# Kernel tuning notes

Hardware: AMD Instinct MI355X
Metric: run time of the kernel (lower is better)

The kernel has to match this reference:

```python
import jax, jax.numpy as jnp
import numpy as np

N = 100000
E = 1600000
IN_C = 128
OUT_C = 32
HEADS = 4
NEG_SLOPE = 0.2


def setup_inputs() -> dict:
    key = jax.random.key(0)
    k1, k2, k3, k4, k5 = jax.random.split(key, 5)
    x = jax.random.normal(k1, (N, IN_C), dtype=jnp.float32)
    edge_index = jax.random.randint(k2, (2, E), 0, N, dtype=jnp.int64)
    # Xavier-ish scaled params
    W = jax.random.normal(k3, (OUT_C * HEADS, IN_C), dtype=jnp.float32) * (1.414 * np.sqrt(2.0 / (IN_C + OUT_C * HEADS)))
    att_l = jax.random.normal(k4, (1, HEADS, OUT_C), dtype=jnp.float32) * 0.1
    att_r = jax.random.normal(k5, (1, HEADS, OUT_C), dtype=jnp.float32) * 0.1
    bias = jnp.zeros((OUT_C * HEADS,), dtype=jnp.float32)
    return {"x": x, "edge_index": edge_index, "W": W, "att_l": att_l, "att_r": att_r, "bias": bias}


def reference(x, edge_index, W, att_l, att_r, bias):
    row, col = edge_index[0], edge_index[1]
    # per-node projection: [N, H, C]
    x_proj = (x @ W.T).reshape(N, HEADS, OUT_C)
    x_i = x_proj[row]          # [E, H, C] gather by source
    x_j = x_proj[col]          # [E, H, C] gather by target
    alpha = (x_i * att_l).sum(-1) + (x_j * att_r).sum(-1)   # [E, H]
    alpha = jnp.where(alpha >= 0, alpha, NEG_SLOPE * alpha)  # leaky_relu
    # edge softmax grouped by row (faithful: plain exp, eps=1e-16)
    alpha_exp = jnp.exp(alpha)
    denom = jax.ops.segment_sum(alpha_exp, row, num_segments=N)  # [N, H]
    alpha = alpha_exp / (denom[row] + 1e-16)
    # weighted scatter-add over all heads at once: [N, H, C]
    out = jax.ops.segment_sum(x_j * alpha[:, :, None], row, num_segments=N)
    out = out.reshape(N, HEADS * OUT_C) + bias
    return out
```

## Files before the change

kernel.cpp:

```cpp
#include <hip/hip_runtime.h>
#include <hip/hip_fp16.h>


constexpr float NEG_SLOPE = 0.2f;
constexpr int TILE_ROWS = 64;
constexpr int SLAB = 2048;
constexpr int EPB = 8192;
constexpr int NB_PAD = 2048;
constexpr int FBMAX = 256;

typedef __attribute__((ext_vector_type(8))) short short8;
typedef __attribute__((ext_vector_type(4))) float f32x4;

__device__ inline short f2bf(float f) {
    unsigned u = __float_as_uint(f);
    return (short)((u + 0x7fffu + ((u >> 16) & 1u)) >> 16);
}

__global__ __launch_bounds__(256) void k_prep(const float* __restrict__ W,
                                              const float* __restrict__ attl,
                                              const float* __restrict__ attr,
                                              short* __restrict__ Wa) {
    int blk = blockIdx.x;
    int t = threadIdx.x;
    if (blk < 64) {
        int i = blk * 256 + t;
        Wa[i] = f2bf(W[i]);
    } else if (blk == 64) {
        for (int s = t; s < 1024; s += 256) {
            int which = s >> 9;
            int h = (s >> 7) & 3;
            int k = s & 127;
            const float* att = which ? attr : attl;
            float acc = 0.f;
#pragma unroll 8
            for (int c = 0; c < 32; ++c)
                acc += att[h * 32 + c] * W[(h * 32 + c) * 128 + k];
            Wa[(128 + which * 4 + h) * 128 + k] = f2bf(acc);
        }
    } else {
        int i = (blk - 65) * 256 + t;
        if (i < 1024) Wa[136 * 128 + i] = 0;
    }
}

__global__ __launch_bounds__(512) void k_fg(const float* __restrict__ x,
                                            const short* __restrict__ Wa,
                                            const int* __restrict__ ei,
                                            __half* __restrict__ xph,
                                            float* __restrict__ l,
                                            float* __restrict__ r,
                                            unsigned int* __restrict__ slab,
                                            int* __restrict__ starts,
                                            int N, int E, int NB, int FB) {
    __shared__ __align__(16) char smem[49152];
    __shared__ int s_wsum[8];
    int t = threadIdx.x;
    int lane = t & 63, wv = t >> 6;

    if ((int)blockIdx.x < FB) {
        int* s_hist = (int*)smem;
        int* s_cur  = (int*)(smem + 8192);
        unsigned int* s_stage = (unsigned int*)(smem + 16384);

        int fb = blockIdx.x;
        int e0 = fb * EPB;
        int ecnt = min(EPB, E - e0);
        bool full = (ecnt == EPB) && ((E & 3) == 0);

        for (int i = t; i < NB_PAD; i += 512) s_hist[i] = 0;
        __syncthreads();

        const int* rows = ei;
        const int* cols = ei + E;

        if (full) {
            const int4* r4 = (const int4*)rows + (e0 >> 2);
#pragma unroll
            for (int k = 0; k < 4; ++k) {
                int4 ra = r4[k * 512 + t];
                atomicAdd(&s_hist[ra.x >> 6], 1);
                atomicAdd(&s_hist[ra.y >> 6], 1);
                atomicAdd(&s_hist[ra.z >> 6], 1);
                atomicAdd(&s_hist[ra.w >> 6], 1);
            }
        } else {
            for (int j = t; j < ecnt; j += 512)
                atomicAdd(&s_hist[rows[e0 + j] >> 6], 1);
        }
        __syncthreads();

        int b0 = t * 4;
        int c0 = s_hist[b0], c1 = s_hist[b0 + 1], c2 = s_hist[b0 + 2], c3 = s_hist[b0 + 3];
        int p = c0 + c1 + c2 + c3;
        int v = p;
#pragma unroll
        for (int off = 1; off < 64; off <<= 1) {
            int u = __shfl_up(v, off);
            if (lane >= off) v += u;
        }
        if (lane == 63) s_wsum[wv] = v;
        __syncthreads();
        if (t == 0) {
            int run = 0;
#pragma unroll
            for (int w = 0; w < 8; ++w) { int tmp = s_wsum[w]; s_wsum[w] = run; run += tmp; }
        }
        __syncthreads();
        int base = s_wsum[wv] + (v - p);
        int e1 = base + c0, e2 = e1 + c1, e3 = e2 + c2;
        s_hist[b0] = base; s_hist[b0 + 1] = e1; s_hist[b0 + 2] = e2; s_hist[b0 + 3] = e3;
        s_cur[b0] = base;  s_cur[b0 + 1] = e1;  s_cur[b0 + 2] = e2;  s_cur[b0 + 3] = e3;
        size_t sb = (size_t)fb * (NB + 1);
        if (b0 + 0 <= NB) starts[sb + b0 + 0] = base;
        if (b0 + 1 <= NB) starts[sb + b0 + 1] = e1;
        if (b0 + 2 <= NB) starts[sb + b0 + 2] = e2;
        if (b0 + 3 <= NB) starts[sb + b0 + 3] = e3;
        __syncthreads();

        if (full) {
            const int4* r4 = (const int4*)rows + (e0 >> 2);
            const int4* c4 = (const int4*)cols + (e0 >> 2);
#pragma unroll
            for (int k = 0; k < 4; ++k) {
                int4 ra = r4[k * 512 + t];
                int4 ca = c4[k * 512 + t];
                int pos;
                pos = atomicAdd(&s_cur[ra.x >> 6], 1);
                s_stage[pos] = ((unsigned int)ca.x << 6) | (unsigned int)(ra.x & 63);
                pos = atomicAdd(&s_cur[ra.y >> 6], 1);
                s_stage[pos] = ((unsigned int)ca.y << 6) | (unsigned int)(ra.y & 63);
                pos = atomicAdd(&s_cur[ra.z >> 6], 1);
                s_stage[pos] = ((unsigned int)ca.z << 6) | (unsigned int)(ra.z & 63);
                pos = atomicAdd(&s_cur[ra.w >> 6], 1);
                s_stage[pos] = ((unsigned int)ca.w << 6) | (unsigned int)(ra.w & 63);
            }
        } else {
            for (int j = t; j < ecnt; j += 512) {
                int rr = rows[e0 + j], cc = cols[e0 + j];
                int pos = atomicAdd(&s_cur[rr >> 6], 1);
                s_stage[pos] = ((unsigned int)cc << 6) | (unsigned int)(rr & 63);
            }
        }
        __syncthreads();

        uint4* dst = (uint4*)(slab + (size_t)fb * EPB);
        const uint4* src = (const uint4*)s_stage;
        int n4 = (ecnt + 3) >> 2;
        for (int i = t; i < n4; i += 512) dst[i] = src[i];
        return;
    }

    short* s_wa = (short*)smem;
    {
        const short8* g = (const short8*)Wa;
        short8* s = (short8*)s_wa;
        for (int i = t; i < 144 * 16; i += 512) {
            int row = i >> 4, k8 = i & 15;
            s[row * 17 + k8] = g[i];
        }
    }
    __syncthreads();

    int li = lane & 15, quad = lane >> 4;
    int gb = blockIdx.x - FB;
    int base = gb * 128 + wv * 16;

    f32x4 acc[9];
#pragma unroll
    for (int nt = 0; nt < 9; ++nt) acc[nt] = (f32x4){0.f, 0.f, 0.f, 0.f};

    int anode = base + li;
    bool avalid = anode < N;
    const float4* x4 = (const float4*)x;
    const short8* wb8 = (const short8*)s_wa;

#pragma unroll
    for (int kc = 0; kc < 4; ++kc) {
        float4 p0 = make_float4(0.f, 0.f, 0.f, 0.f), p1 = p0;
        if (avalid) {
            p0 = x4[(size_t)anode * 32 + kc * 8 + quad * 2];
            p1 = x4[(size_t)anode * 32 + kc * 8 + quad * 2 + 1];
        }
        short8 a;
        a[0] = f2bf(p0.x); a[1] = f2bf(p0.y); a[2] = f2bf(p0.z); a[3] = f2bf(p0.w);
        a[4] = f2bf(p1.x); a[5] = f2bf(p1.y); a[6] = f2bf(p1.z); a[7] = f2bf(p1.w);
#pragma unroll
        for (int nt = 0; nt < 9; ++nt) {
            short8 b = wb8[(nt * 16 + li) * 17 + kc * 4 + quad];
            acc[nt] = __builtin_amdgcn_mfma_f32_16x16x32_bf16(a, b, acc[nt], 0, 0, 0);
        }
    }

#pragma unroll
    for (int j = 0; j < 4; ++j) {
        int node = base + quad * 4 + j;
        if (node >= N) continue;
        if (li < 4)      l[node * 4 + li] = acc[8][j];
        else if (li < 8) r[node * 4 + li - 4] = acc[8][j];
    }

    __syncthreads();
    __half* s_out = (__half*)s_wa;
#pragma unroll
    for (int j = 0; j < 4; ++j) {
        int nl = wv * 16 + quad * 4 + j;
#pragma unroll
        for (int nt = 0; nt < 8; ++nt)
            s_out[nl * 136 + nt * 16 + li] = __float2half(acc[nt][j]);
    }
    __syncthreads();
    {
        int nl = t >> 2, seg = t & 3;
        int node = gb * 128 + nl;
        if (node < N) {
            const short8* sr = (const short8*)s_wa;
            short8* xp8 = (short8*)xph;
#pragma unroll
            for (int q = 0; q < 4; ++q)
                xp8[(size_t)node * 16 + seg * 4 + q] = sr[nl * 17 + seg * 4 + q];
        }
    }
}

__global__ __launch_bounds__(512) void k_tile(const int* __restrict__ starts,
                                              const unsigned int* __restrict__ slab,
                                              const float* __restrict__ l,
                                              const float* __restrict__ r,
                                              const __half* __restrict__ xph,
                                              const float* __restrict__ bias,
                                              float* __restrict__ out,
                                              int N, int NB, int FB) {
    __shared__ unsigned int s_packed[SLAB];
    __shared__ int s_col[SLAB];
    __shared__ __half s_w[SLAB * 4];
    __shared__ float s_dsum[TILE_ROWS * 4];
    __shared__ float s_l[TILE_ROWS * 4];
    __shared__ int s_start[TILE_ROWS + 1];
    __shared__ int s_cursor[TILE_ROWS];
    __shared__ int s_cnt[TILE_ROWS];
    __shared__ int s_fbase[FBMAX];
    __shared__ int s_foff[FBMAX + 1];
    __shared__ int s_w4[4];

    int b = blockIdx.x;
    int base = b * TILE_ROWS;
    int t = threadIdx.x;
    int lane = t & 63, wv = t >> 6;
    int rows = min(TILE_ROWS, N - base);

    if (t < TILE_ROWS) s_cnt[t] = 0;
    if (t < rows * 4) s_l[t] = l[base * 4 + t];

    int myc = 0;
    if (t < FB) {
        const int* sp = starts + (size_t)t * (NB + 1) + b;
        int a0 = sp[0], a1 = sp[1];
        s_fbase[t] = a0;
        myc = a1 - a0;
    }
    int v = 0;
    if (t < 256) {
        v = myc;
#pragma unroll
        for (int off = 1; off < 64; off <<= 1) {
            int u = __shfl_up(v, off);
            if (lane >= off) v += u;
        }
        if (lane == 63) s_w4[wv] = v;
    }
    __syncthreads();
    if (t == 0) {
        int run = 0;
#pragma unroll
        for (int w = 0; w < 4; ++w) { int tmp = s_w4[w]; s_w4[w] = run; run += tmp; }
        s_foff[0] = 0;
    }
    __syncthreads();
    if (t < 256) s_foff[t + 1] = v + s_w4[wv];
    __syncthreads();
    int tot = s_foff[FB];
    if (tot > SLAB) tot = SLAB;

    for (int i = t; i < tot; i += 512) {
        int lo = 0, hi = FB;
        while (hi - lo > 1) {
            int mid = (lo + hi) >> 1;
            if (s_foff[mid] <= i) lo = mid; else hi = mid;
        }
        unsigned int p = slab[(size_t)lo * EPB + s_fbase[lo] + (i - s_foff[lo])];
        s_packed[i] = p;
        atomicAdd(&s_cnt[p & 63], 1);
    }
    __syncthreads();

    if (t < 64) {
        int c = s_cnt[t];
        int vv = c;
#pragma unroll
        for (int off = 1; off < 64; off <<= 1) {
            int u = __shfl_up(vv, off);
            if (t >= off) vv += u;
        }
        s_start[t + 1] = vv;
        if (t == 0) s_start[0] = 0;
        s_cursor[t] = vv - c;
    }
    __syncthreads();

    {
        int row_[4], col_[4];
        bool val_[4];
#pragma unroll
        for (int s = 0; s < 4; ++s) {
            int i = t + s * 512;
            bool valid = i < tot;
            unsigned int p = valid ? s_packed[i] : 0u;
            row_[s] = (int)(p & 63);
            col_[s] = valid ? (int)(p >> 6) : 0;
            val_[s] = valid;
        }
        float4 rv0 = ((const float4*)r)[col_[0]];
        float4 rv1 = ((const float4*)r)[col_[1]];
        float4 rv2 = ((const float4*)r)[col_[2]];
        float4 rv3 = ((const float4*)r)[col_[3]];
#pragma unroll
        for (int s = 0; s < 4; ++s) {
            if (!val_[s]) continue;
            float4 rv = s == 0 ? rv0 : s == 1 ? rv1 : s == 2 ? rv2 : rv3;
            int row = row_[s];
            int pos = atomicAdd(&s_cursor[row], 1);
            s_col[pos] = col_[s];
            float4 lv = ((const float4*)s_l)[row];
            float w0 = lv.x + rv.x, w1 = lv.y + rv.y;
            float w2 = lv.z + rv.z, w3 = lv.w + rv.w;
            w0 = w0 >= 0.f ? w0 : NEG_SLOPE * w0;
            w1 = w1 >= 0.f ? w1 : NEG_SLOPE * w1;
            w2 = w2 >= 0.f ? w2 : NEG_SLOPE * w2;
            w3 = w3 >= 0.f ? w3 : NEG_SLOPE * w3;
            w0 = __expf(w0); w1 = __expf(w1); w2 = __expf(w2); w3 = __expf(w3);
            ((__half2*)s_w)[pos * 2]     = __floats2half2_rn(w0, w1);
            ((__half2*)s_w)[pos * 2 + 1] = __floats2half2_rn(w2, w3);
        }
    }
    __syncthreads();

    if (t < 256) {
        int row = t >> 2, h = t & 3;
        if (row < rows) {
            int s0 = s_start[row], s1 = s_start[row + 1];
            float d = 0.f;
            for (int i = s0; i < s1; ++i)
                d += __half2float(s_w[i * 4 + h]);
            s_dsum[t] = d;
        }
    }
    __syncthreads();

    int quarter = lane >> 4;
    int li = lane & 15;
    int h = li >> 2;
    const float4* xp4g = (const float4*)xph;

    float4 b0 = ((const float4*)bias)[2 * li];
    float4 b1 = ((const float4*)bias)[2 * li + 1];

    for (int rl = wv; rl < rows; rl += 8) {
        int s0 = s_start[rl], s1 = s_start[rl + 1];
        float a0 = 0.f, a1 = 0.f, a2 = 0.f, a3 = 0.f;
        float a4 = 0.f, a5 = 0.f, a6 = 0.f, a7 = 0.f;
        for (int i = s0 + quarter; i < s1; i += 8) {
            int iB = i + 4;
            bool hB = iB < s1;
            int colA = s_col[i];
            float wA = __half2float(s_w[i * 4 + h]);
            int colB = hB ? s_col[iB] : colA;
            float wB = hB ? __half2float(s_w[iB * 4 + h]) : 0.f;
            float4 rawA = xp4g[(size_t)colA * 16 + li];
            float4 rawB = xp4g[(size_t)colB * 16 + li];
            {
                __half2* hp = (__half2*)&rawA;
                float2 f0 = __half22float2(hp[0]);
                float2 f1 = __half22float2(hp[1]);
                float2 f2 = __half22float2(hp[2]);
                float2 f3 = __half22float2(hp[3]);
                a0 += wA * f0.x; a1 += wA * f0.y;
                a2 += wA * f1.x; a3 += wA * f1.y;
                a4 += wA * f2.x; a5 += wA * f2.y;
                a6 += wA * f3.x; a7 += wA * f3.y;
            }
            {
                __half2* hp = (__half2*)&rawB;
                float2 f0 = __half22float2(hp[0]);
                float2 f1 = __half22float2(hp[1]);
                float2 f2 = __half22float2(hp[2]);
                float2 f3 = __half22float2(hp[3]);
                a0 += wB * f0.x; a1 += wB * f0.y;
                a2 += wB * f1.x; a3 += wB * f1.y;
                a4 += wB * f2.x; a5 += wB * f2.y;
                a6 += wB * f3.x; a7 += wB * f3.y;
            }
        }
        a0 += __shfl_xor(a0, 16); a0 += __shfl_xor(a0, 32);
        a1 += __shfl_xor(a1, 16); a1 += __shfl_xor(a1, 32);
        a2 += __shfl_xor(a2, 16); a2 += __shfl_xor(a2, 32);
        a3 += __shfl_xor(a3, 16); a3 += __shfl_xor(a3, 32);
        a4 += __shfl_xor(a4, 16); a4 += __shfl_xor(a4, 32);
        a5 += __shfl_xor(a5, 16); a5 += __shfl_xor(a5, 32);
        a6 += __shfl_xor(a6, 16); a6 += __shfl_xor(a6, 32);
        a7 += __shfl_xor(a7, 16); a7 += __shfl_xor(a7, 32);
        if (quarter == 0) {
            float inv = 1.f / (s_dsum[rl * 4 + h] + 1e-16f);
            float4 o0, o1;
            o0.x = a0 * inv + b0.x; o0.y = a1 * inv + b0.y;
            o0.z = a2 * inv + b0.z; o0.w = a3 * inv + b0.w;
            o1.x = a4 * inv + b1.x; o1.y = a5 * inv + b1.y;
            o1.z = a6 * inv + b1.z; o1.w = a7 * inv + b1.w;
            ((float4*)out)[(size_t)(base + rl) * 32 + 2 * li] = o0;
            ((float4*)out)[(size_t)(base + rl) * 32 + 2 * li + 1] = o1;
        }
    }
}

extern "C" void kernel_launch(void* const* d_in, const int* in_sizes, int n_in,
                              void* d_out, int out_size, void* d_ws, size_t ws_size,
                              hipStream_t stream) {
    const float* x    = (const float*)d_in[0];
    const int*   ei   = (const int*)d_in[1];
    const float* W    = (const float*)d_in[2];
    const float* attl = (const float*)d_in[3];
    const float* attr = (const float*)d_in[4];
    const float* bias = (const float*)d_in[5];
    int N = in_sizes[0] / 128;
    int E = in_sizes[1] / 2;
    int NB = (N + TILE_ROWS - 1) / TILE_ROWS;
    int FB = (E + EPB - 1) / EPB;

    char* ws = (char*)d_ws;
    __half* xph = (__half*)ws;   ws += (size_t)N * 128 * 2;
    float* l    = (float*)ws;    ws += (size_t)N * 4 * 4;
    float* r    = (float*)ws;    ws += (size_t)N * 4 * 4;
    short* Wa   = (short*)ws;    ws += 144 * 128 * 2;
    int* starts = (int*)ws;      ws += (size_t)FB * (NB + 1) * 4;
    unsigned int* slab = (unsigned int*)ws; ws += (size_t)FB * EPB * 4;

    float* out = (float*)d_out;
    int GB = (N + 127) / 128;

    k_prep<<<69, 256, 0, stream>>>(W, attl, attr, Wa);
    k_fg<<<FB + GB, 512, 0, stream>>>(x, Wa, ei, xph, l, r, slab, starts, N, E, NB, FB);
    k_tile<<<NB, 512, 0, stream>>>(starts, slab, l, r, xph, bias, out, N, NB, FB);
}
```

Measured before the change: 204.5 us.

## Fuse weight prep into fill/GEMM kernel, interleave fill blocks, unroll gather by four

Removes the separate k_prep launch. Every GEMM block now converts W to bf16 in shared memory and computes the attention-projected rows itself. Fill (bucketing) blocks are spread evenly among the GEMM blocks through a stride S instead of all being placed first, so the two kinds of work mix across CUs. The k_tile gather loop now issues four neighbour row loads per iteration instead of two, to raise memory-level parallelism. In exchange, every GEMM block redundantly reads all of W from global memory and computes the projected rows, which adds global traffic and ALU work per block.

```diff
diff --git a/kernel.cpp b/kernel.cpp
--- a/kernel.cpp
+++ b/kernel.cpp
@@ -17,53 +17,31 @@
     return (short)((u + 0x7fffu + ((u >> 16) & 1u)) >> 16);
 }
 
-__global__ __launch_bounds__(256) void k_prep(const float* __restrict__ W,
-                                              const float* __restrict__ attl,
-                                              const float* __restrict__ attr,
-                                              short* __restrict__ Wa) {
-    int blk = blockIdx.x;
-    int t = threadIdx.x;
-    if (blk < 64) {
-        int i = blk * 256 + t;
-        Wa[i] = f2bf(W[i]);
-    } else if (blk == 64) {
-        for (int s = t; s < 1024; s += 256) {
-            int which = s >> 9;
-            int h = (s >> 7) & 3;
-            int k = s & 127;
-            const float* att = which ? attr : attl;
-            float acc = 0.f;
-#pragma unroll 8
-            for (int c = 0; c < 32; ++c)
-                acc += att[h * 32 + c] * W[(h * 32 + c) * 128 + k];
-            Wa[(128 + which * 4 + h) * 128 + k] = f2bf(acc);
-        }
-    } else {
-        int i = (blk - 65) * 256 + t;
-        if (i < 1024) Wa[136 * 128 + i] = 0;
-    }
-}
-
 __global__ __launch_bounds__(512) void k_fg(const float* __restrict__ x,
-                                            const short* __restrict__ Wa,
+                                            const float* __restrict__ W,
+                                            const float* __restrict__ attl,
+                                            const float* __restrict__ attr,
                                             const int* __restrict__ ei,
                                             __half* __restrict__ xph,
                                             float* __restrict__ l,
                                             float* __restrict__ r,
                                             unsigned int* __restrict__ slab,
                                             int* __restrict__ starts,
-                                            int N, int E, int NB, int FB) {
+                                            int N, int E, int NB, int FB, int S) {
     __shared__ __align__(16) char smem[49152];
+    __shared__ float s_att[256];
     __shared__ int s_wsum[8];
     int t = threadIdx.x;
     int lane = t & 63, wv = t >> 6;
-
-    if ((int)blockIdx.x < FB) {
+    int b = blockIdx.x;
+    bool isfill = (b % S == 0) && (b / S < FB);
+
+    if (isfill) {
         int* s_hist = (int*)smem;
         int* s_cur  = (int*)(smem + 8192);
         unsigned int* s_stage = (unsigned int*)(smem + 16384);
 
-        int fb = blockIdx.x;
+        int fb = b / S;
         int e0 = fb * EPB;
         int ecnt = min(EPB, E - e0);
         bool full = (ecnt == EPB) && ((E & 3) == 0);
@@ -152,18 +130,33 @@
     }
 
     short* s_wa = (short*)smem;
-    {
-        const short8* g = (const short8*)Wa;
-        short8* s = (short8*)s_wa;
-        for (int i = t; i < 144 * 16; i += 512) {
-            int row = i >> 4, k8 = i & 15;
-            s[row * 17 + k8] = g[i];
-        }
+    if (t < 128)       s_att[t] = attl[t];
+    else if (t < 256)  s_att[t] = attr[t - 128];
+    for (int i = t; i < 128 * 128; i += 512) {
+        int row = i >> 7, col = i & 127;
+        s_wa[row * 136 + col] = f2bf(W[i]);
+    }
+    for (int i = t; i < 1024; i += 512) {
+        int row = 136 + (i >> 7), col = i & 127;
+        s_wa[row * 136 + col] = 0;
+    }
+    __syncthreads();
+#pragma unroll
+    for (int s = 0; s < 2; ++s) {
+        int e = t + s * 512;
+        int which = e >> 9;
+        int h = (e >> 7) & 3;
+        int k = e & 127;
+        float acc = 0.f;
+#pragma unroll 8
+        for (int c = 0; c < 32; ++c)
+            acc += s_att[which * 128 + h * 32 + c] * W[(h * 32 + c) * 128 + k];
+        s_wa[(128 + which * 4 + h) * 136 + k] = f2bf(acc);
     }
     __syncthreads();
 
     int li = lane & 15, quad = lane >> 4;
-    int gb = blockIdx.x - FB;
+    int gb = b - min((b + S - 1) / S, FB);
     int base = gb * 128 + wv * 16;
 
     f32x4 acc[9];
@@ -187,8 +180,8 @@
         a[4] = f2bf(p1.x); a[5] = f2bf(p1.y); a[6] = f2bf(p1.z); a[7] = f2bf(p1.w);
 #pragma unroll
         for (int nt = 0; nt < 9; ++nt) {
-            short8 b = wb8[(nt * 16 + li) * 17 + kc * 4 + quad];
-            acc[nt] = __builtin_amdgcn_mfma_f32_16x16x32_bf16(a, b, acc[nt], 0, 0, 0);
+            short8 bfrag = wb8[(nt * 16 + li) * 17 + kc * 4 + quad];
+            acc[nt] = __builtin_amdgcn_mfma_f32_16x16x32_bf16(a, bfrag, acc[nt], 0, 0, 0);
         }
     }
 
@@ -369,37 +362,38 @@
         int s0 = s_start[rl], s1 = s_start[rl + 1];
         float a0 = 0.f, a1 = 0.f, a2 = 0.f, a3 = 0.f;
         float a4 = 0.f, a5 = 0.f, a6 = 0.f, a7 = 0.f;
-        for (int i = s0 + quarter; i < s1; i += 8) {
-            int iB = i + 4;
-            bool hB = iB < s1;
-            int colA = s_col[i];
-            float wA = __half2float(s_w[i * 4 + h]);
-            int colB = hB ? s_col[iB] : colA;
-            float wB = hB ? __half2float(s_w[iB * 4 + h]) : 0.f;
-            float4 rawA = xp4g[(size_t)colA * 16 + li];
-            float4 rawB = xp4g[(size_t)colB * 16 + li];
-            {
-                __half2* hp = (__half2*)&rawA;
-                float2 f0 = __half22float2(hp[0]);
-                float2 f1 = __half22float2(hp[1]);
-                float2 f2 = __half22float2(hp[2]);
-                float2 f3 = __half22float2(hp[3]);
-                a0 += wA * f0.x; a1 += wA * f0.y;
-                a2 += wA * f1.x; a3 += wA * f1.y;
-                a4 += wA * f2.x; a5 += wA * f2.y;
-                a6 += wA * f3.x; a7 += wA * f3.y;
+        for (int i0 = s0 + quarter; i0 < s1; i0 += 16) {
+            int i1 = i0 + 4, i2 = i0 + 8, i3 = i0 + 12;
+            bool v1 = i1 < s1, v2 = i2 < s1, v3 = i3 < s1;
+            int c0 = s_col[i0];
+            int c1 = v1 ? s_col[i1] : c0;
+            int c2 = v2 ? s_col[i2] : c0;
+            int c3 = v3 ? s_col[i3] : c0;
+            float w0 = __half2float(s_w[i0 * 4 + h]);
+            float w1 = v1 ? __half2float(s_w[i1 * 4 + h]) : 0.f;
+            float w2 = v2 ? __half2float(s_w[i2 * 4 + h]) : 0.f;
+            float w3 = v3 ? __half2float(s_w[i3 * 4 + h]) : 0.f;
+            float4 r0 = xp4g[(size_t)c0 * 16 + li];
+            float4 r1 = xp4g[(size_t)c1 * 16 + li];
+            float4 r2 = xp4g[(size_t)c2 * 16 + li];
+            float4 r3 = xp4g[(size_t)c3 * 16 + li];
+#define ACC8(raw, w)                                         \
+            {                                                \
+                __half2* hp = (__half2*)&(raw);              \
+                float2 f0 = __half22float2(hp[0]);           \
+                float2 f1 = __half22float2(hp[1]);           \
+                float2 f2 = __half22float2(hp[2]);           \
+                float2 f3 = __half22float2(hp[3]);           \
+                a0 += (w) * f0.x; a1 += (w) * f0.y;          \
+                a2 += (w) * f1.x; a3 += (w) * f1.y;          \
+                a4 += (w) * f2.x; a5 += (w) * f2.y;          \
+                a6 += (w) * f3.x; a7 += (w) * f3.y;          \
             }
-            {
-                __half2* hp = (__half2*)&rawB;
-                float2 f0 = __half22float2(hp[0]);
-                float2 f1 = __half22float2(hp[1]);
-                float2 f2 = __half22float2(hp[2]);
-                float2 f3 = __half22float2(hp[3]);
-                a0 += wB * f0.x; a1 += wB * f0.y;
-                a2 += wB * f1.x; a3 += wB * f1.y;
-                a4 += wB * f2.x; a5 += wB * f2.y;
-                a6 += wB * f3.x; a7 += wB * f3.y;
-            }
+            ACC8(r0, w0);
+            ACC8(r1, w1);
+            ACC8(r2, w2);
+            ACC8(r3, w3);
+#undef ACC8
         }
         a0 += __shfl_xor(a0, 16); a0 += __shfl_xor(a0, 32);
         a1 += __shfl_xor(a1, 16); a1 += __shfl_xor(a1, 32);
@@ -440,14 +434,15 @@
     __half* xph = (__half*)ws;   ws += (size_t)N * 128 * 2;
     float* l    = (float*)ws;    ws += (size_t)N * 4 * 4;
     float* r    = (float*)ws;    ws += (size_t)N * 4 * 4;
-    short* Wa   = (short*)ws;    ws += 144 * 128 * 2;
     int* starts = (int*)ws;      ws += (size_t)FB * (NB + 1) * 4;
     unsigned int* slab = (unsigned int*)ws; ws += (size_t)FB * EPB * 4;
 
     float* out = (float*)d_out;
     int GB = (N + 127) / 128;
-
-    k_prep<<<69, 256, 0, stream>>>(W, attl, attr, Wa);
-    k_fg<<<FB + GB, 512, 0, stream>>>(x, Wa, ei, xph, l, r, slab, starts, N, E, NB, FB);
+    int TOT = FB + GB;
+    int S = TOT / FB; if (S < 1) S = 1;
+
+    k_fg<<<TOT, 512, 0, stream>>>(x, W, attl, attr, ei, xph, l, r, slab, starts,
+                                  N, E, NB, FB, S);
     k_tile<<<NB, 512, 0, stream>>>(starts, slab, l, r, xph, bias, out, N, NB, FB);
 }
```

Result: no change. 206.4 us (+1.0%).
